# Optimization experiments

Hardware: AMD Instinct MI355X
Metric: run time of the kernel (lower is better)

## Reference

```python
import jax, jax.numpy as jnp
import numpy as np

N_BINS = ((1, 1), (2, 2), (4, 4), (8, 8))  # SPP pyramid; sum(ph*pw) = 85


def _pool_one_scale(x, ph, pw):
    """Max-pool x [B,H,W,C] into ph x pw bins.

    Bin i covers rows [i*hs, (i+1)*hs) except the last, which extends to H
    (matching the TF layer's floor-step + last-bin-extends semantics).
    Returns [B, ph*pw*C] flattened in (bin_i, bin_j, channel) order.
    """
    B, H, W, C = x.shape
    hs, ws = H // ph, W // pw
    # pool over height
    main = x[:, : (ph - 1) * hs].reshape(B, ph - 1, hs, W, C).max(axis=2)
    last = x[:, (ph - 1) * hs :].max(axis=1, keepdims=True)
    xh = jnp.concatenate([main, last], axis=1)  # [B, ph, W, C]
    # pool over width
    main = xh[:, :, : (pw - 1) * ws].reshape(B, ph, pw - 1, ws, C).max(axis=3)
    last = xh[:, :, (pw - 1) * ws :].max(axis=2, keepdims=True)
    out = jnp.concatenate([main, last], axis=2)  # [B, ph, pw, C]
    return out.reshape(B, ph * pw * C)


def setup_inputs() -> dict:
    key = jax.random.key(0)
    x = jax.random.normal(key, (32, 64, 64, 512), dtype=jnp.float32)
    return {"x": x}


def reference(x):
    # concat multi-scale pooled embeddings -> [B, sum(ph*pw)*C]
    return jnp.concatenate([_pool_one_scale(x, ph, pw) for ph, pw in N_BINS], axis=1)
```

## Files before the change

### kernel.cpp

```cpp
#include <hip/hip_runtime.h>
#include <hip/hip_bf16.h>
#include <math.h>


#define C_F4 128
#define ROW_OUT 43520
#define S8_OFF 10752
#define S4_OFF 2560
#define S2_OFF 512

static __device__ __forceinline__ float4 f4max(float4 a, float4 b) {
    float4 r;
    r.x = fmaxf(a.x, b.x);
    r.y = fmaxf(a.y, b.y);
    r.z = fmaxf(a.z, b.z);
    r.w = fmaxf(a.w, b.w);
    return r;
}

__global__ __launch_bounds__(256) void spp_pool84(const float* __restrict__ x,
                                                  float* __restrict__ out) {
    const int blk = blockIdx.x;
    const int b   = blk >> 4;
    const int rem = blk & 15;
    const int i4  = rem >> 2;
    const int j4  = rem & 3;
    const int tid = threadIdx.x;
    const int s   = tid >> 7;
    const int c4  = tid & 127;

    const int row0 = i4 * 16 + s * 8;
    const float4* src = reinterpret_cast<const float4*>(x)
                      + (size_t)((b * 64 + row0) * 64 + j4 * 16) * C_F4 + c4;

    float4 m0 = src[0];
    float4 m1 = src[8 * 128];
    #pragma unroll 2
    for (int h = 0; h < 8; ++h) {
        #pragma unroll
        for (int w = 0; w < 8; ++w) {
            if (h == 0 && w == 0) continue;
            m0 = f4max(m0, src[h * 8192 + w * 128]);
            m1 = f4max(m1, src[h * 8192 + (w + 8) * 128]);
        }
    }

    float* row = out + (size_t)b * ROW_OUT;
    const int i8 = 2 * i4 + s;
    const int j8 = 2 * j4;
    reinterpret_cast<float4*>(row + S8_OFF + (i8 * 8 + j8) * 512)[c4]     = m0;
    reinterpret_cast<float4*>(row + S8_OFF + (i8 * 8 + j8 + 1) * 512)[c4] = m1;

    __shared__ float4 ls[2][128];
    ls[s][c4] = f4max(m0, m1);
    __syncthreads();
    if (s == 0) {
        float4 v4 = f4max(ls[0][c4], ls[1][c4]);
        reinterpret_cast<float4*>(row + S4_OFF + (i4 * 4 + j4) * 512)[c4] = v4;
    }
}

__global__ __launch_bounds__(512) void spp_tail(float* __restrict__ out) {
    const int b   = blockIdx.x;
    const int tid = threadIdx.x;
    const int q   = tid >> 7;
    const int c4  = tid & 127;
    const int i2  = q >> 1;
    const int j2  = q & 1;

    float* row = out + (size_t)b * ROW_OUT;
    const float4* p4 = reinterpret_cast<const float4*>(row + S4_OFF) + c4;

    float4 m = p4[((2 * i2) * 4 + 2 * j2) * C_F4];
    m = f4max(m, p4[((2 * i2) * 4 + 2 * j2 + 1) * C_F4]);
    m = f4max(m, p4[((2 * i2 + 1) * 4 + 2 * j2) * C_F4]);
    m = f4max(m, p4[((2 * i2 + 1) * 4 + 2 * j2 + 1) * C_F4]);

    reinterpret_cast<float4*>(row + S2_OFF + q * 512)[c4] = m;

    __shared__ float4 ls[4][128];
    ls[q][c4] = m;
    __syncthreads();
    if (q == 0) {
        float4 v1 = f4max(f4max(ls[0][c4], ls[1][c4]),
                          f4max(ls[2][c4], ls[3][c4]));
        reinterpret_cast<float4*>(row)[c4] = v1;
    }
}

extern "C" void kernel_launch(void* const* d_in, const int* in_sizes, int n_in,
                              void* d_out, int out_size, void* d_ws, size_t ws_size,
                              hipStream_t stream) {
    const float* x = (const float*)d_in[0];
    float* out = (float*)d_out;

    spp_pool84<<<512, 256, 0, stream>>>(x, out);
    spp_tail<<<32, 512, 0, stream>>>(out);
}
```

Before: 47.41 us.

## Fuse tail pooling into main kernel via last-block atomic counter, nontemporal loads

Folds the 2x2 and 1x1 pyramid levels into the main pooling kernel. Each block bumps a per-batch atomic counter, and the last of the 16 blocks for a batch reads the 4x4 results and writes the coarser levels, which removes the second kernel launch. Input loads also switch to nontemporal builtins to avoid polluting the cache with streamed data. The change adds a memset per call plus threadfence and atomic overhead, and the memset is an extra stream operation that may show up in the timing.

```diff
diff --git a/kernel.cpp b/kernel.cpp
--- a/kernel.cpp
+++ b/kernel.cpp
@@ -9,8 +9,10 @@
 #define S4_OFF 2560
 #define S2_OFF 512
 
-static __device__ __forceinline__ float4 f4max(float4 a, float4 b) {
-    float4 r;
+typedef float vf4 __attribute__((ext_vector_type(4)));
+
+static __device__ __forceinline__ vf4 vmax(vf4 a, vf4 b) {
+    vf4 r;
     r.x = fmaxf(a.x, b.x);
     r.y = fmaxf(a.y, b.y);
     r.z = fmaxf(a.z, b.z);
@@ -18,8 +20,9 @@
     return r;
 }
 
-__global__ __launch_bounds__(256) void spp_pool84(const float* __restrict__ x,
-                                                  float* __restrict__ out) {
+__global__ __launch_bounds__(256) void spp_fused(const float* __restrict__ x,
+                                                 float* __restrict__ out,
+                                                 int* __restrict__ cnt) {
     const int blk = blockIdx.x;
     const int b   = blk >> 4;
     const int rem = blk & 15;
@@ -30,61 +33,61 @@
     const int c4  = tid & 127;
 
     const int row0 = i4 * 16 + s * 8;
-    const float4* src = reinterpret_cast<const float4*>(x)
-                      + (size_t)((b * 64 + row0) * 64 + j4 * 16) * C_F4 + c4;
+    const vf4* src = reinterpret_cast<const vf4*>(x)
+                   + (size_t)((b * 64 + row0) * 64 + j4 * 16) * C_F4 + c4;
 
-    float4 m0 = src[0];
-    float4 m1 = src[8 * 128];
+    vf4 m0 = __builtin_nontemporal_load(src);
+    vf4 m1 = __builtin_nontemporal_load(src + 8 * 128);
     #pragma unroll 2
     for (int h = 0; h < 8; ++h) {
         #pragma unroll
         for (int w = 0; w < 8; ++w) {
             if (h == 0 && w == 0) continue;
-            m0 = f4max(m0, src[h * 8192 + w * 128]);
-            m1 = f4max(m1, src[h * 8192 + (w + 8) * 128]);
+            m0 = vmax(m0, __builtin_nontemporal_load(src + h * 8192 + w * 128));
+            m1 = vmax(m1, __builtin_nontemporal_load(src + h * 8192 + (w + 8) * 128));
         }
     }
 
     float* row = out + (size_t)b * ROW_OUT;
     const int i8 = 2 * i4 + s;
     const int j8 = 2 * j4;
-    reinterpret_cast<float4*>(row + S8_OFF + (i8 * 8 + j8) * 512)[c4]     = m0;
-    reinterpret_cast<float4*>(row + S8_OFF + (i8 * 8 + j8 + 1) * 512)[c4] = m1;
+    reinterpret_cast<vf4*>(row + S8_OFF + (i8 * 8 + j8) * 512)[c4]     = m0;
+    reinterpret_cast<vf4*>(row + S8_OFF + (i8 * 8 + j8 + 1) * 512)[c4] = m1;
 
-    __shared__ float4 ls[2][128];
-    ls[s][c4] = f4max(m0, m1);
+    __shared__ vf4 ls[2][128];
+    ls[s][c4] = vmax(m0, m1);
     __syncthreads();
     if (s == 0) {
-        float4 v4 = f4max(ls[0][c4], ls[1][c4]);
-        reinterpret_cast<float4*>(row + S4_OFF + (i4 * 4 + j4) * 512)[c4] = v4;
+        vf4 v4 = vmax(ls[0][c4], ls[1][c4]);
+        reinterpret_cast<vf4*>(row + S4_OFF + (i4 * 4 + j4) * 512)[c4] = v4;
     }
-}
 
-__global__ __launch_bounds__(512) void spp_tail(float* __restrict__ out) {
-    const int b   = blockIdx.x;
-    const int tid = threadIdx.x;
-    const int q   = tid >> 7;
-    const int c4  = tid & 127;
-    const int i2  = q >> 1;
-    const int j2  = q & 1;
-
-    float* row = out + (size_t)b * ROW_OUT;
-    const float4* p4 = reinterpret_cast<const float4*>(row + S4_OFF) + c4;
-
-    float4 m = p4[((2 * i2) * 4 + 2 * j2) * C_F4];
-    m = f4max(m, p4[((2 * i2) * 4 + 2 * j2 + 1) * C_F4]);
-    m = f4max(m, p4[((2 * i2 + 1) * 4 + 2 * j2) * C_F4]);
-    m = f4max(m, p4[((2 * i2 + 1) * 4 + 2 * j2 + 1) * C_F4]);
-
-    reinterpret_cast<float4*>(row + S2_OFF + q * 512)[c4] = m;
-
-    __shared__ float4 ls[4][128];
-    ls[q][c4] = m;
+    __shared__ int lastflag;
+    __threadfence();
     __syncthreads();
-    if (q == 0) {
-        float4 v1 = f4max(f4max(ls[0][c4], ls[1][c4]),
-                          f4max(ls[2][c4], ls[3][c4]));
-        reinterpret_cast<float4*>(row)[c4] = v1;
+    if (tid == 0)
+        lastflag = (atomicAdd(&cnt[b], 1) == 15) ? 1 : 0;
+    __syncthreads();
+    if (lastflag) {
+        __threadfence();
+        const vf4* p4 = reinterpret_cast<const vf4*>(row + S4_OFF) + c4;
+        vf4 acc;
+        #pragma unroll
+        for (int k = 0; k < 2; ++k) {
+            const int q  = 2 * s + k;
+            const int i2 = q >> 1;
+            const int j2 = q & 1;
+            vf4 m =        p4[((2 * i2)     * 4 + 2 * j2)     * C_F4];
+            m = vmax(m,    p4[((2 * i2)     * 4 + 2 * j2 + 1) * C_F4]);
+            m = vmax(m,    p4[((2 * i2 + 1) * 4 + 2 * j2)     * C_F4]);
+            m = vmax(m,    p4[((2 * i2 + 1) * 4 + 2 * j2 + 1) * C_F4]);
+            reinterpret_cast<vf4*>(row + S2_OFF + q * 512)[c4] = m;
+            acc = (k == 0) ? m : vmax(acc, m);
+        }
+        ls[s][c4] = acc;
+        __syncthreads();
+        if (s == 0)
+            reinterpret_cast<vf4*>(row)[c4] = vmax(ls[0][c4], ls[1][c4]);
     }
 }
 
@@ -93,7 +96,8 @@
                               hipStream_t stream) {
     const float* x = (const float*)d_in[0];
     float* out = (float*)d_out;
+    int* cnt = (int*)d_ws;
 
-    spp_pool84<<<512, 256, 0, stream>>>(x, out);
-    spp_tail<<<32, 512, 0, stream>>>(out);
+    hipMemsetAsync(cnt, 0, 32 * sizeof(int), stream);
+    spp_fused<<<512, 256, 0, stream>>>(x, out, cnt);
 }
```

Result: slower. 131.4 us (+177.1%).
